# Kernel optimization log

Measured on AMD Instinct MI355X. Metric: run time of the kernel, lower is better.

The kernel has to match this reference:

```python
import jax, jax.numpy as jnp
import numpy as np

MARGIN = 0.075
CONF_THRESHOLD = 0.2


def setup_inputs() -> dict:
    key = jax.random.key(0)
    k1, k2, k3 = jax.random.split(key, 3)
    N, D = 32768, 256
    embeddings = jax.random.normal(k1, (N, D), dtype=jnp.float32)
    tags = jax.random.randint(k2, (N,), 0, 500, dtype=jnp.int64)
    confidences = jax.random.uniform(k3, (N,), dtype=jnp.float32)
    return {"embeddings": embeddings, "tags": tags, "confidences": confidences}


def _safe_sqrt(sq):
    # gradient-safe sqrt: zero at sq<=0 (matches d(0)=0, avoids NaN in vjp)
    pos = sq > 0
    return jnp.where(pos, jnp.sqrt(jnp.where(pos, sq, 1.0)), 0.0)


def _triplet_hard_mining(emb, labels):
    n = emb.shape[0]
    # pairwise euclidean distances (cdist p=2)
    sq_norm = jnp.sum(emb * emb, axis=1)  # [n]
    sq = sq_norm[:, None] + sq_norm[None, :] - 2.0 * (emb @ emb.T)
    dist = _safe_sqrt(jnp.maximum(sq, 0.0))  # [n, n]

    same = labels[:, None] == labels[None, :]
    eye = jnp.eye(n, dtype=bool)
    pos_mask = same & ~eye
    neg_mask = ~same

    inf = jnp.float32(jnp.inf)
    hard_pos = jnp.max(jnp.where(pos_mask, dist, -inf), axis=1)  # [n]
    neg_min = jnp.min(jnp.where(neg_mask, dist, inf), axis=1)    # [n]
    # semi-hard negatives: neg dists strictly greater than hardest positive
    shn_mask = neg_mask & (dist > hard_pos[:, None])
    shn_min = jnp.min(jnp.where(shn_mask, dist, inf), axis=1)
    hard_neg = jnp.where(jnp.isfinite(shn_min), shn_min, neg_min)

    valid = jnp.any(pos_mask, axis=1) & jnp.any(neg_mask, axis=1)
    per_anchor = jax.nn.relu(hard_pos - hard_neg + MARGIN)
    per_anchor = jnp.where(valid, per_anchor, 0.0)
    cnt = jnp.sum(valid.astype(jnp.float32))
    # if no valid anchors (also covers <2 unique labels), loss is 0
    return jnp.where(cnt > 0, jnp.sum(per_anchor) / jnp.maximum(cnt, 1.0), 0.0)


def reference(embeddings, tags, confidences):
    n = embeddings.shape[0]
    top_k = int(CONF_THRESHOLD * n)
    _, idx = jax.lax.top_k(confidences, top_k)
    emb = embeddings[idx]
    labels = tags[idx]
    return _triplet_hard_mining(emb, labels)
```

## Files before the change

### kernel.cpp

```cpp
#include <hip/hip_runtime.h>
#include <math.h>

#define D 256
#define MARGIN 0.075f
#define MAXM 96
#define NBIN 8192

typedef __bf16 bf8_t __attribute__((ext_vector_type(8)));
typedef float f4_t __attribute__((ext_vector_type(4)));
typedef unsigned long long ull;

#define AS1 __attribute__((address_space(1)))
#define AS3 __attribute__((address_space(3)))
static __device__ __forceinline__ void gload_lds16(const void* g, void* s) {
    __builtin_amdgcn_global_load_lds((const AS1 unsigned int*)g, (AS3 unsigned int*)s, 16, 0, 0);
}

#define ALOADU(p) __hip_atomic_load((p), __ATOMIC_RELAXED, __HIP_MEMORY_SCOPE_AGENT)
#define ASTOREU(p, v) __hip_atomic_store((p), (v), __ATOMIC_RELAXED, __HIP_MEMORY_SCOPE_AGENT)

#define VDRAIN() asm volatile("s_waitcnt vmcnt(0)" ::: "memory")


static __device__ __forceinline__ unsigned short f2bf(float x) {
    unsigned u = __float_as_uint(x);
    unsigned r = (u + 0x7fffu + ((u >> 16) & 1u)) >> 16;
    return (unsigned short)r;
}

static __device__ __forceinline__ float dec_min(unsigned cm) {
    return (cm == 0u) ? __builtin_inff() : __uint_as_float(~cm);
}

static __device__ __forceinline__ float rmin16(float v) {
    int s;
    s = __builtin_amdgcn_update_dpp(__float_as_int(v), __float_as_int(v), 0x101, 0xF, 0xF, false);
    v = fminf(v, __int_as_float(s));
    s = __builtin_amdgcn_update_dpp(__float_as_int(v), __float_as_int(v), 0x102, 0xF, 0xF, false);
    v = fminf(v, __int_as_float(s));
    s = __builtin_amdgcn_update_dpp(__float_as_int(v), __float_as_int(v), 0x104, 0xF, 0xF, false);
    v = fminf(v, __int_as_float(s));
    s = __builtin_amdgcn_update_dpp(__float_as_int(v), __float_as_int(v), 0x108, 0xF, 0xF, false);
    v = fminf(v, __int_as_float(s));
    return v;
}

__global__ __launch_bounds__(1024) void k_histsel(const float* __restrict__ conf, int n,
                                                  unsigned* __restrict__ ctrl, int ksel,
                                                  int* __restrict__ idx_sel,
                                                  ull* __restrict__ cand) {
    __shared__ __align__(16) unsigned shist[NBIN];
    __shared__ __align__(16) char aux[16384];
    unsigned* part = (unsigned*)aux;
    int t = threadIdx.x;

    for (int b = t; b < NBIN; b += 1024) shist[b] = 0u;
    __syncthreads();
    for (int i = t; i < n; i += 1024) {
        unsigned b = __float_as_uint(conf[i]) >> 17;
        if (b > NBIN - 1u) b = NBIN - 1u;
        atomicAdd(&shist[b], 1u);
    }
    __syncthreads();

    unsigned k = (unsigned)ksel;
    unsigned loc[8];
    unsigned s = 0;
    #pragma unroll
    for (int b = 0; b < 8; b++) { loc[b] = shist[t * 8 + b]; s += loc[b]; }
    part[t] = s;
    __syncthreads();
    for (int off = 1; off < 1024; off <<= 1) {
        unsigned v = (t + off < 1024) ? part[t + off] : 0u;
        __syncthreads();
        part[t] += v;
        __syncthreads();
    }
    __shared__ int schunk;
    __shared__ unsigned sbin, sneed, scgt;
    if (part[t] >= k && (t == 1023 || part[t + 1] < k)) schunk = t;
    __syncthreads();
    int c = schunk;
    if (t == c) {
        unsigned cum = (c == 1023) ? 0u : part[c + 1];
        int bin = 0; unsigned rem = 1;
        #pragma unroll
        for (int b = 7; b >= 0; b--) {
            unsigned h = loc[b];
            if (cum + h >= k) { bin = c * 8 + b; rem = k - cum; break; }
            cum += h;
        }
        sbin = (unsigned)bin; sneed = rem; scgt = k - rem;
    }
    __syncthreads();
    unsigned b16 = sbin, need = sneed, cgt = scgt;

    int i = blockIdx.x * 1024 + t;
    if (i < n) {
        unsigned u = __float_as_uint(conf[i]);
        unsigned tb = u >> 17;
        if (tb > NBIN - 1u) tb = NBIN - 1u;
        if (tb > b16) {
            unsigned pos = atomicAdd(&ctrl[5], 1u);
            idx_sel[pos] = i;
        } else if (tb == b16) {
            unsigned pos = atomicAdd(&ctrl[6], 1u);
            ASTOREU(&cand[pos], ((ull)u << 32) | (unsigned)i);
        }
    }
    VDRAIN();
    __syncthreads();
    __shared__ int lastf;
    if (t == 0) lastf = (atomicAdd(&ctrl[11], 1u) == gridDim.x - 1) ? 1 : 0;
    __syncthreads();
    if (!lastf) return;

    ull* scand = (ull*)aux;
    int M = (int)atomicAdd(&ctrl[6], 0u);
    if (M <= 2048) {
        for (int j = t; j < M; j += 1024) scand[j] = ALOADU(&cand[j]);
        __syncthreads();
        for (int j = t; j < M; j += 1024) {
            ull cj = scand[j];
            unsigned uj = (unsigned)(cj >> 32);
            unsigned rank = 0;
            for (int m = 0; m < M; m++) {
                ull cm = scand[m];
                unsigned um = (unsigned)(cm >> 32);
                if (um > uj || (um == uj && cm < cj)) rank++;
            }
            if (rank < need) idx_sel[cgt + rank] = (int)(unsigned)(cj & 0xFFFFFFFFu);
        }
    } else {
        for (int j = t; j < M; j += 1024) {
            ull cj = ALOADU(&cand[j]);
            unsigned uj = (unsigned)(cj >> 32);
            unsigned rank = 0;
            for (int m = 0; m < M; m++) {
                ull cm = ALOADU(&cand[m]);
                unsigned um = (unsigned)(cm >> 32);
                if (um > uj || (um == uj && cm < cj)) rank++;
            }
            if (rank < need) idx_sel[cgt + rank] = (int)(unsigned)(cj & 0xFFFFFFFFu);
        }
    }
}

__global__ __launch_bounds__(256) void k_gather(const float* __restrict__ emb,
                                                const int* __restrict__ tags,
                                                const int* __restrict__ idx_sel,
                                                int ksel, int np,
                                                unsigned short* __restrict__ ebf,
                                                float* __restrict__ sqn,
                                                int* __restrict__ lsel,
                                                unsigned* __restrict__ labhist,
                                                int* __restrict__ members) {
    int j = blockIdx.x * 4 + (threadIdx.x >> 6);
    int t = threadIdx.x & 63;
    if (j < ksel) {
        int src = idx_sel[j];
        float4 v = *(const float4*)&emb[(size_t)src * D + t * 4];
        ushort4 o;
        o.x = f2bf(v.x); o.y = f2bf(v.y); o.z = f2bf(v.z); o.w = f2bf(v.w);
        *(ushort4*)&ebf[(size_t)j * D + t * 4] = o;
        float s = v.x * v.x + v.y * v.y + v.z * v.z + v.w * v.w;
        for (int off = 32; off > 0; off >>= 1) s += __shfl_down(s, off);
        if (t == 0) {
            int lab = tags[src];
            sqn[j] = s; lsel[j] = lab;
            unsigned slot = atomicAdd(&labhist[lab], 1u);
            if (slot < MAXM) members[lab * MAXM + slot] = j;
        }
    } else if (j < np) {
        ushort4 z = {0, 0, 0, 0};
        *(ushort4*)&ebf[(size_t)j * D + t * 4] = z;
        if (t == 0) { sqn[j] = __builtin_inff(); lsel[j] = -1; }
    }
}

__global__ __launch_bounds__(256) void k_hardpos(const unsigned short* __restrict__ ebf,
                                                 const float* __restrict__ sqn,
                                                 const int* __restrict__ members,
                                                 const unsigned* __restrict__ labhist,
                                                 unsigned* __restrict__ hp_g) {
    int L = blockIdx.x;
    int t = threadIdx.x;
    int m = (int)labhist[L];
    if (m > MAXM) m = MAXM;
    if (m < 2) return;

    __shared__ unsigned short rows[MAXM * 256];
    __shared__ float lsqn[MAXM];
    __shared__ unsigned hpl[MAXM];
    __shared__ int ridx[MAXM];

    for (int a = t; a < m; a += 256) {
        int r = members[L * MAXM + a];
        ridx[a] = r; lsqn[a] = sqn[r]; hpl[a] = 0u;
    }
    __syncthreads();
    for (int e = t * 8; e < m * 256; e += 256 * 8) {
        int a = e >> 8, c = e & 255;
        *(uint4*)&rows[a * 256 + c] = *(const uint4*)&ebf[(size_t)ridx[a] * D + c];
    }
    __syncthreads();

    int npair = m * (m - 1) / 2;
    for (int pidx = t; pidx < npair; pidx += 256) {
        int a = 0, rem = pidx;
        while (rem >= m - 1 - a) { rem -= m - 1 - a; a++; }
        int b = a + 1 + rem;
        const unsigned* ra = (const unsigned*)&rows[a * 256];
        const unsigned* rb = (const unsigned*)&rows[b * 256];
        float dot = 0.f;
        #pragma unroll 8
        for (int c = 0; c < 128; c++) {
            unsigned ua = ra[c], ub = rb[c];
            float a0 = __uint_as_float(ua << 16);
            float a1 = __uint_as_float(ua & 0xFFFF0000u);
            float b0 = __uint_as_float(ub << 16);
            float b1 = __uint_as_float(ub & 0xFFFF0000u);
            dot = fmaf(a0, b0, dot);
            dot = fmaf(a1, b1, dot);
        }
        float dsq = fmaxf(lsqn[a] + lsqn[b] - 2.f * dot, 0.f);
        unsigned bits = __float_as_uint(dsq);
        atomicMax(&hpl[a], bits);
        atomicMax(&hpl[b], bits);
    }
    __syncthreads();
    for (int a = t; a < m; a += 256) hp_g[ridx[a]] = hpl[a];
}

__global__ __launch_bounds__(256, 3) void k_fused(const unsigned short* __restrict__ Ebf,
                                                  const float* __restrict__ sqn,
                                                  const int* __restrict__ lsel,
                                                  const unsigned* __restrict__ hp_g,
                                                  unsigned* __restrict__ nm_g,
                                                  unsigned* __restrict__ shn_g,
                                                  int np, int nb, int ksel) {
    int rem = blockIdx.x, bi = 0;
    while (rem >= nb - bi) { rem -= nb - bi; bi++; }
    int bj = bi + rem;
    int i0 = bi * 128, j0 = bj * 128;
    bool diag = (bi == bj);

    __shared__ __align__(16) char smem[32768];
    char* ldsA = smem;
    char* ldsB = smem + 16384;

    int t = threadIdx.x;
    int w = t >> 6, l = t & 63;
    int wm = w & 1, wn = w >> 1;
    int lr = l & 15, lq = l >> 4;
    int r7 = lr & 7, rh = lr >> 3;

    int dr = l >> 3;
    int sg = (l & 7) ^ dr;
    const unsigned short* gA = Ebf + (size_t)(i0 + dr) * D + sg * 8;
    const unsigned short* gB = Ebf + (size_t)(j0 + dr) * D + sg * 8;

    f4_t zero = {0.f, 0.f, 0.f, 0.f};
    f4_t acc[4][4];
    #pragma unroll
    for (int p = 0; p < 4; p++)
        #pragma unroll
        for (int q = 0; q < 4; q++) acc[p][q] = zero;

    for (int k0 = 0; k0 < D; k0 += 64) {
        #pragma unroll
        for (int c = 0; c < 4; c++) {
            int R0 = w * 32 + c * 8;
            gload_lds16(gA + (size_t)R0 * D + k0, ldsA + R0 * 128);
            gload_lds16(gB + (size_t)R0 * D + k0, ldsB + R0 * 128);
        }
        __syncthreads();
        #pragma unroll
        for (int ks8 = 0; ks8 < 8; ks8 += 4) {
            bf8_t a[4], b[4];
            #pragma unroll
            for (int p = 0; p < 4; p++) {
                int off = ((wm * 8 + p * 2 + rh) << 10) + ((r7 * 8 + ((ks8 + lq) ^ r7)) << 4);
                a[p] = *(const bf8_t*)(ldsA + off);
            }
            #pragma unroll
            for (int q = 0; q < 4; q++) {
                int off = ((wn * 8 + q * 2 + rh) << 10) + ((r7 * 8 + ((ks8 + lq) ^ r7)) << 4);
                b[q] = *(const bf8_t*)(ldsB + off);
            }
            #pragma unroll
            for (int p = 0; p < 4; p++)
                #pragma unroll
                for (int q = 0; q < 4; q++)
                    acc[p][q] = __builtin_amdgcn_mfma_f32_16x16x32_bf16(a[p], b[q], acc[p][q], 0, 0, 0);
        }
        __syncthreads();
    }

    float* sqnA = (float*)smem;
    float* sqnB = sqnA + 128;
    int* labA = (int*)(sqnB + 128);
    int* labB = labA + 128;
    float* hpA2 = (float*)(labB + 128);
    float* hpB2 = hpA2 + 128;
    if (t < 128) {
        sqnA[t] = sqn[i0 + t];
        labA[t] = lsel[i0 + t];
        hpA2[t] = __uint_as_float(hp_g[i0 + t]);
    } else {
        int u = t - 128;
        sqnB[u] = sqn[j0 + u];
        labB[u] = lsel[j0 + u];
        hpB2[u] = __uint_as_float(hp_g[j0 + u]);
    }
    __syncthreads();

    const float INF = __builtin_inff();
    float dsq[4][4][4];
    int colL[4], ljv[4];
    float sBv[4];
    #pragma unroll
    for (int q = 0; q < 4; q++) {
        colL[q] = wn * 64 + q * 16 + lr;
        ljv[q] = labB[colL[q]];
        sBv[q] = sqnB[colL[q]];
    }
    #pragma unroll
    for (int p = 0; p < 4; p++) {
        #pragma unroll
        for (int r = 0; r < 4; r++) {
            int rowL = wm * 64 + p * 16 + lq * 4 + r;
            float smi = sqnA[rowL];
            #pragma unroll
            for (int q = 0; q < 4; q++)
                dsq[p][q][r] = fmaxf(smi + sBv[q] - 2.f * acc[p][q][r], 0.f);
        }
    }

    #pragma unroll
    for (int p = 0; p < 4; p++) {
        #pragma unroll
        for (int r = 0; r < 4; r++) {
            int rowL = wm * 64 + p * 16 + lq * 4 + r;
            int li = labA[rowL];
            float hpr = hpA2[rowL];
            float nmv = INF, smv = INF;
            #pragma unroll
            for (int q = 0; q < 4; q++) {
                float d = dsq[p][q][r];
                if (ljv[q] != li) {
                    nmv = fminf(nmv, d);
                    if (d > hpr) smv = fminf(smv, d);
                }
            }
            nmv = rmin16(nmv);
            smv = rmin16(smv);
            if (lr == 0) {
                if (nmv < INF) atomicMax(&nm_g[i0 + rowL], ~__float_as_uint(nmv));
                if (smv < INF) atomicMax(&shn_g[i0 + rowL], ~__float_as_uint(smv));
            }
        }
    }

    if (!diag) {
        #pragma unroll
        for (int q = 0; q < 4; q++) {
            int lj = ljv[q];
            float hpc = hpB2[colL[q]];
            float nmv = INF, smv = INF;
            #pragma unroll
            for (int p = 0; p < 4; p++)
                #pragma unroll
                for (int r = 0; r < 4; r++) {
                    int rowL = wm * 64 + p * 16 + lq * 4 + r;
                    float d = dsq[p][q][r];
                    if (labA[rowL] != lj) {
                        nmv = fminf(nmv, d);
                        if (d > hpc) smv = fminf(smv, d);
                    }
                }
            nmv = fminf(nmv, __shfl_xor(nmv, 16));
            nmv = fminf(nmv, __shfl_xor(nmv, 32));
            smv = fminf(smv, __shfl_xor(smv, 16));
            smv = fminf(smv, __shfl_xor(smv, 32));
            if (lq == 0) {
                if (nmv < INF) atomicMax(&nm_g[j0 + colL[q]], ~__float_as_uint(nmv));
                if (smv < INF) atomicMax(&shn_g[j0 + colL[q]], ~__float_as_uint(smv));
            }
        }
    }
}

__global__ __launch_bounds__(256) void k_loss(const unsigned* __restrict__ hp,
                                              const unsigned* __restrict__ nm,
                                              const unsigned* __restrict__ shn,
                                              const int* __restrict__ lsel,
                                              const unsigned* __restrict__ labhist,
                                              int ksel, float* __restrict__ fsums,
                                              unsigned* __restrict__ ctrl,
                                              float* __restrict__ out) {
    __shared__ float ssum[256], scnt[256];
    int t = threadIdx.x;
    int i = blockIdx.x * 256 + t;
    float sum = 0.f, cnt = 0.f;
    if (i < ksel) {
        int li = lsel[i];
        unsigned h = labhist[li];
        bool valid = (h >= 2u) && ((unsigned)ksel > h);
        if (valid) {
            float hp2 = __uint_as_float(hp[i]);
            float nm2 = dec_min(nm[i]);
            float sh2 = dec_min(shn[i]);
            float hn2 = isinf(sh2) ? nm2 : sh2;
            sum = fmaxf(sqrtf(hp2) - sqrtf(hn2) + MARGIN, 0.f);
            cnt = 1.f;
        }
    }
    ssum[t] = sum; scnt[t] = cnt;
    __syncthreads();
    for (int off = 128; off > 0; off >>= 1) {
        if (t < off) { ssum[t] += ssum[t + off]; scnt[t] += scnt[t + off]; }
        __syncthreads();
    }
    if (t == 0) {
        atomicAdd(&fsums[0], ssum[0]);
        atomicAdd(&fsums[1], scnt[0]);
        VDRAIN();
        unsigned done = atomicAdd(&ctrl[7], 1u);
        if (done == gridDim.x - 1) {
            float s = atomicAdd(&fsums[0], 0.f);
            float c = atomicAdd(&fsums[1], 0.f);
            out[0] = (c > 0.f) ? (s / fmaxf(c, 1.f)) : 0.f;
        }
    }
}

__global__ void k_wsfail(float* out, float code) { out[0] = code; }

static inline size_t align_up(size_t x, size_t a) { return (x + a - 1) & ~(a - 1); }

extern "C" void kernel_launch(void* const* d_in, const int* in_sizes, int n_in,
                              void* d_out, int out_size, void* d_ws, size_t ws_size,
                              hipStream_t stream) {
    const float* emb  = (const float*)d_in[0];
    const int*   tags = (const int*)d_in[1];
    const float* conf = (const float*)d_in[2];
    float* out = (float*)d_out;

    int n = in_sizes[2];
    int ksel = (int)(0.2 * (double)n);
    int np = ((ksel + 127) / 128) * 128;
    int nb = np / 128;
    int nlab = 512;

    size_t off = 0;
    size_t o_ctrl = off; off = align_up(off + 32 * sizeof(unsigned), 256);
    size_t o_fs   = off; off = align_up(off + 8 * sizeof(float), 256);
    size_t o_lh   = off; off = align_up(off + (size_t)nlab * 4, 256);
    size_t o_hp   = off; off = align_up(off + (size_t)np * 4, 256);
    size_t o_nm   = off; off = align_up(off + (size_t)np * 4, 256);
    size_t o_shn  = off; off = align_up(off + (size_t)np * 4, 256);
    size_t zero_bytes = off;
    size_t o_idx  = off; off = align_up(off + (size_t)ksel * 4, 256);
    size_t o_cand = off; off = align_up(off + (size_t)n * 8, 256);
    size_t o_mem  = off; off = align_up(off + (size_t)nlab * MAXM * 4, 256);
    size_t o_lab  = off; off = align_up(off + (size_t)np * 4, 256);
    size_t o_sqn  = off; off = align_up(off + (size_t)np * 4, 256);
    size_t o_ebf  = off; off = align_up(off + (size_t)np * D * 2, 256);

    if (ws_size < off) {
        k_wsfail<<<1, 1, 0, stream>>>(out, -(float)(ws_size >> 20));
        return;
    }

    char* ws = (char*)d_ws;
    unsigned*       ctrl    = (unsigned*)(ws + o_ctrl);
    float*          fsums   = (float*)(ws + o_fs);
    unsigned*       labhist = (unsigned*)(ws + o_lh);
    unsigned*       hp_g    = (unsigned*)(ws + o_hp);
    unsigned*       nm_g    = (unsigned*)(ws + o_nm);
    unsigned*       shn_g   = (unsigned*)(ws + o_shn);
    int*            idx_sel = (int*)(ws + o_idx);
    ull*            cand    = (ull*)(ws + o_cand);
    int*            members = (int*)(ws + o_mem);
    int*            lsel    = (int*)(ws + o_lab);
    float*          sqn     = (float*)(ws + o_sqn);
    unsigned short* ebf     = (unsigned short*)(ws + o_ebf);

    hipMemsetAsync(d_ws, 0, zero_bytes, stream);
    int nhb = (n + 1023) / 1024;
    k_histsel<<<nhb, 1024, 0, stream>>>(conf, n, ctrl, ksel, idx_sel, cand);
    k_gather<<<np / 4, 256, 0, stream>>>(emb, tags, idx_sel, ksel, np, ebf, sqn, lsel,
                                         labhist, members);
    k_hardpos<<<512, 256, 0, stream>>>(ebf, sqn, members, labhist, hp_g);
    int ntri = nb * (nb + 1) / 2;
    k_fused<<<ntri, 256, 0, stream>>>(ebf, sqn, lsel, hp_g, nm_g, shn_g, np, nb, ksel);
    k_loss<<<(ksel + 255) / 256, 256, 0, stream>>>(hp_g, nm_g, shn_g, lsel, labhist,
                                                   ksel, fsums, ctrl, out);
}
```

Measured before the change: 172.6 us.

## Fuse gather and hard-positive kernels into one per-label kernel

```diff
diff --git a/kernel.cpp b/kernel.cpp
--- a/kernel.cpp
+++ b/kernel.cpp
@@ -146,62 +146,72 @@
     }
 }
 
-__global__ __launch_bounds__(256) void k_gather(const float* __restrict__ emb,
-                                                const int* __restrict__ tags,
-                                                const int* __restrict__ idx_sel,
-                                                int ksel, int np,
-                                                unsigned short* __restrict__ ebf,
-                                                float* __restrict__ sqn,
-                                                int* __restrict__ lsel,
-                                                unsigned* __restrict__ labhist,
-                                                int* __restrict__ members) {
-    int j = blockIdx.x * 4 + (threadIdx.x >> 6);
-    int t = threadIdx.x & 63;
-    if (j < ksel) {
-        int src = idx_sel[j];
-        float4 v = *(const float4*)&emb[(size_t)src * D + t * 4];
-        ushort4 o;
-        o.x = f2bf(v.x); o.y = f2bf(v.y); o.z = f2bf(v.z); o.w = f2bf(v.w);
-        *(ushort4*)&ebf[(size_t)j * D + t * 4] = o;
-        float s = v.x * v.x + v.y * v.y + v.z * v.z + v.w * v.w;
-        for (int off = 32; off > 0; off >>= 1) s += __shfl_down(s, off);
-        if (t == 0) {
-            int lab = tags[src];
-            sqn[j] = s; lsel[j] = lab;
-            unsigned slot = atomicAdd(&labhist[lab], 1u);
-            if (slot < MAXM) members[lab * MAXM + slot] = j;
-        }
-    } else if (j < np) {
-        ushort4 z = {0, 0, 0, 0};
-        *(ushort4*)&ebf[(size_t)j * D + t * 4] = z;
-        if (t == 0) { sqn[j] = __builtin_inff(); lsel[j] = -1; }
-    }
-}
-
-__global__ __launch_bounds__(256) void k_hardpos(const unsigned short* __restrict__ ebf,
-                                                 const float* __restrict__ sqn,
-                                                 const int* __restrict__ members,
-                                                 const unsigned* __restrict__ labhist,
-                                                 unsigned* __restrict__ hp_g) {
+__global__ __launch_bounds__(256) void k_gatherpos(const float* __restrict__ emb,
+                                                   const int* __restrict__ tags,
+                                                   const int* __restrict__ idx_sel,
+                                                   int ksel, int np,
+                                                   unsigned short* __restrict__ ebf,
+                                                   float* __restrict__ sqn,
+                                                   int* __restrict__ lsel,
+                                                   unsigned* __restrict__ labhist,
+                                                   unsigned* __restrict__ hp_g) {
+    int t = threadIdx.x;
+
+    int ngrp = np / 4;
+    for (int g = blockIdx.x; g < ngrp; g += gridDim.x) {
+        int j = g * 4 + (t >> 6);
+        int lane = t & 63;
+        if (j < ksel) {
+            int src = idx_sel[j];
+            float4 v = *(const float4*)&emb[(size_t)src * D + lane * 4];
+            ushort4 o;
+            o.x = f2bf(v.x); o.y = f2bf(v.y); o.z = f2bf(v.z); o.w = f2bf(v.w);
+            *(ushort4*)&ebf[(size_t)j * D + lane * 4] = o;
+            float s = v.x * v.x + v.y * v.y + v.z * v.z + v.w * v.w;
+            for (int off = 32; off > 0; off >>= 1) s += __shfl_down(s, off);
+            if (lane == 0) {
+                sqn[j] = s; lsel[j] = tags[src];
+                atomicAdd(&labhist[tags[src]], 1u);
+            }
+        } else {
+            ushort4 z = {0, 0, 0, 0};
+            *(ushort4*)&ebf[(size_t)j * D + (t & 63) * 4] = z;
+            if ((t & 63) == 0) { sqn[j] = __builtin_inff(); lsel[j] = -1; }
+        }
+    }
+
     int L = blockIdx.x;
-    int t = threadIdx.x;
-    int m = (int)labhist[L];
-    if (m > MAXM) m = MAXM;
-    if (m < 2) return;
-
     __shared__ unsigned short rows[MAXM * 256];
     __shared__ float lsqn[MAXM];
     __shared__ unsigned hpl[MAXM];
-    __shared__ int ridx[MAXM];
-
-    for (int a = t; a < m; a += 256) {
-        int r = members[L * MAXM + a];
-        ridx[a] = r; lsqn[a] = sqn[r]; hpl[a] = 0u;
-    }
-    __syncthreads();
-    for (int e = t * 8; e < m * 256; e += 256 * 8) {
-        int a = e >> 8, c = e & 255;
-        *(uint4*)&rows[a * 256 + c] = *(const uint4*)&ebf[(size_t)ridx[a] * D + c];
+    __shared__ int memj[MAXM];
+    __shared__ int memsrc[MAXM];
+    __shared__ int scnt_;
+
+    if (t == 0) scnt_ = 0;
+    __syncthreads();
+    for (int j = t; j < ksel; j += 256) {
+        int src = idx_sel[j];
+        if (tags[src] == L) {
+            int slot = atomicAdd(&scnt_, 1);
+            if (slot < MAXM) { memj[slot] = j; memsrc[slot] = src; }
+        }
+    }
+    __syncthreads();
+    int m = scnt_;
+    if (m > MAXM) m = MAXM;
+    if (m < 2) return;
+
+    int w = t >> 6, l = t & 63;
+    for (int a = w; a < m; a += 4) {
+        int src = memsrc[a];
+        float4 v = *(const float4*)&emb[(size_t)src * D + l * 4];
+        ushort4 o;
+        o.x = f2bf(v.x); o.y = f2bf(v.y); o.z = f2bf(v.z); o.w = f2bf(v.w);
+        *(ushort4*)&rows[a * 256 + l * 4] = o;
+        float s = v.x * v.x + v.y * v.y + v.z * v.z + v.w * v.w;
+        for (int off = 32; off > 0; off >>= 1) s += __shfl_down(s, off);
+        if (l == 0) { lsqn[a] = s; hpl[a] = 0u; }
     }
     __syncthreads();
 
@@ -229,7 +239,7 @@
         atomicMax(&hpl[b], bits);
     }
     __syncthreads();
-    for (int a = t; a < m; a += 256) hp_g[ridx[a]] = hpl[a];
+    for (int a = t; a < m; a += 256) hp_g[memj[a]] = hpl[a];
 }
 
 __global__ __launch_bounds__(256, 3) void k_fused(const unsigned short* __restrict__ Ebf,
@@ -463,7 +473,6 @@
     size_t zero_bytes = off;
     size_t o_idx  = off; off = align_up(off + (size_t)ksel * 4, 256);
     size_t o_cand = off; off = align_up(off + (size_t)n * 8, 256);
-    size_t o_mem  = off; off = align_up(off + (size_t)nlab * MAXM * 4, 256);
     size_t o_lab  = off; off = align_up(off + (size_t)np * 4, 256);
     size_t o_sqn  = off; off = align_up(off + (size_t)np * 4, 256);
     size_t o_ebf  = off; off = align_up(off + (size_t)np * D * 2, 256);
@@ -482,7 +491,6 @@
     unsigned*       shn_g   = (unsigned*)(ws + o_shn);
     int*            idx_sel = (int*)(ws + o_idx);
     ull*            cand    = (ull*)(ws + o_cand);
-    int*            members = (int*)(ws + o_mem);
     int*            lsel    = (int*)(ws + o_lab);
     float*          sqn     = (float*)(ws + o_sqn);
     unsigned short* ebf     = (unsigned short*)(ws + o_ebf);
@@ -490,9 +498,8 @@
     hipMemsetAsync(d_ws, 0, zero_bytes, stream);
     int nhb = (n + 1023) / 1024;
     k_histsel<<<nhb, 1024, 0, stream>>>(conf, n, ctrl, ksel, idx_sel, cand);
-    k_gather<<<np / 4, 256, 0, stream>>>(emb, tags, idx_sel, ksel, np, ebf, sqn, lsel,
-                                         labhist, members);
-    k_hardpos<<<512, 256, 0, stream>>>(ebf, sqn, members, labhist, hp_g);
+    k_gatherpos<<<nlab, 256, 0, stream>>>(emb, tags, idx_sel, ksel, np, ebf, sqn,
+                                          lsel, labhist, hp_g);
     int ntri = nb * (nb + 1) / 2;
     k_fused<<<ntri, 256, 0, stream>>>(ebf, sqn, lsel, hp_g, nm_g, shn_g, np, nb, ksel);
     k_loss<<<(ksel + 255) / 256, 256, 0, stream>>>(hp_g, nm_g, shn_g, lsel, labhist,
```

Result: slower. 181.2 us (+5.0%).
